# Kernel optimization log

Measured on AMD Instinct MI355X. Metric: run time of the kernel, lower is better.

## Reference

```python
import jax, jax.numpy as jnp
import numpy as np

N, D, C = 8192, 128, 64
MARGIN = 0.5


def setup_inputs() -> dict:
    key = jax.random.key(0)
    k1, k2 = jax.random.split(key)
    embedings = jax.random.normal(k1, (N, D), dtype=jnp.float32)
    targets = jax.random.randint(k2, (N,), 0, C, dtype=jnp.int32)
    return {"embedings": embedings, "targets": targets}


def _triplet_terms(x, targets):
    # pairwise squared distances, faithful to pairwise_distances(y=None):
    xn = jnp.sum(x * x, axis=1)                       # [N]
    d = xn[:, None] + xn[None, :] - 2.0 * (x @ x.T)   # [N, N]
    d = jnp.clip(d - jnp.diagonal(d)[None, :], 0.0)

    same = targets[:, None] == targets[None, :]        # [N, N] bool
    diff = ~same
    BIG = jnp.float32(1e30)
    g_pos = jnp.argmax(jnp.where(same, d, -BIG), axis=1)  # farthest same-class (global idx)
    g_neg = jnp.argmin(jnp.where(diff, d, BIG), axis=1)   # closest other-class (global idx)

    # Faithful to source bug: the mined index is the POSITION WITHIN THE
    # SAME/DIFF-CLASS SUBSET (np.argsort on the masked slice), which the
    # original then uses to index the full embedding batch.
    cum_same = jnp.cumsum(same.astype(jnp.int32), axis=1)
    cum_diff = jnp.cumsum(diff.astype(jnp.int32), axis=1)
    p_pos = jnp.take_along_axis(cum_same, g_pos[:, None], axis=1)[:, 0] - 1
    p_neg = jnp.take_along_axis(cum_diff, g_neg[:, None], axis=1)[:, 0] - 1

    anchors = x
    positives = x[p_pos]
    negatives = x[p_neg]

    valid = (jnp.sum(same, axis=1) > 1) & (jnp.sum(diff, axis=1) >= 1)
    vf = valid.astype(x.dtype)                         # [N]
    vcount = jnp.sum(vf)

    ap = jnp.sum((anchors - positives) ** 2, axis=1)
    an = jnp.sum((anchors - negatives) ** 2, axis=1)
    npd = jnp.sum((positives - negatives) ** 2, axis=1)

    tl = jax.nn.relu(ap - an + MARGIN) * vf
    non_zero = jnp.sum((tl > 0).astype(jnp.int32))
    triplet_term = jnp.where(
        non_zero == 0,
        jnp.sum(tl) / vcount,                                   # mean over valid rows
        jnp.sum(tl) / jnp.maximum(non_zero, 1).astype(x.dtype),  # sum(tl / non_zero)
    )

    l1 = lambda v: jnp.sum(jnp.abs(v) * vf[:, None]) / vcount
    sparse_term = (l1(anchors) + l1(positives) + l1(negatives)) / 3.0

    pairwise_term = jax.nn.relu(jnp.sum((ap - an - npd) * vf) / vcount)

    ap_mean = jnp.sum(ap * vf) / vcount
    an_mean = jnp.sum(an * vf) / vcount
    return triplet_term, sparse_term, pairwise_term, vcount, ap_mean, an_mean


def reference(embedings, targets):
    return _triplet_terms(embedings, targets)
```

## Files before the change

kernel.cpp:

```cpp
#include <hip/hip_runtime.h>
#include <float.h>
#include <stdint.h>

#define NROWS 8192
#define DIM 128
#define MARGIN 0.5f
#define NCHUNK (NROWS / 64)
#define SCH 16
#define RLB (NROWS / 8)

typedef __attribute__((ext_vector_type(8))) short short8;
typedef __attribute__((ext_vector_type(4))) float floatx4;

__device__ __forceinline__ void load_lds16(const void* g, void* l) {
    __builtin_amdgcn_global_load_lds(
        (const __attribute__((address_space(1))) unsigned int*)g,
        (__attribute__((address_space(3))) unsigned int*)l, 16, 0, 0);
}

__device__ __forceinline__ unsigned rne_pack(float v0, float v1) {
    unsigned u0 = __float_as_uint(v0), u1 = __float_as_uint(v1);
    unsigned r0 = (u0 + 0x7fffu + ((u0 >> 16) & 1u)) >> 16;
    unsigned r1 = (u1 + 0x7fffu + ((u1 >> 16) & 1u)) & 0xffff0000u;
    return r0 | r1;
}

__global__ __launch_bounds__(256) void prep_kernel(const float* __restrict__ x,
                                                   const int* __restrict__ tgt,
                                                   uint4* __restrict__ fragH,
                                                   float* __restrict__ xn,
                                                   float* __restrict__ l1n,
                                                   int* __restrict__ pre,
                                                   int* __restrict__ cc,
                                                   float* __restrict__ gacc,
                                                   int* __restrict__ cnt) {
    __shared__ int cntS[NCHUNK][64];
    const int b = blockIdx.x;
    if (b < NROWS / 16) {
        float (*sums)[17] = (float (*)[17])cntS;
        float (*suml)[17] = ((float (*)[17])cntS) + 16;
        const int t = threadIdx.x;
        const int s = t >> 6, lane = t & 63;
        const int rloc = lane & 15;
        const int k0 = s * 32 + (lane >> 4) * 8;
        const float* xr = x + (size_t)(b * 16 + rloc) * DIM + k0;
        float4 va = *(const float4*)xr, vb = *(const float4*)(xr + 4);
        float vv[8] = {va.x, va.y, va.z, va.w, vb.x, vb.y, vb.z, vb.w};
        unsigned h[4];
        float ss = 0.f, ll = 0.f;
        #pragma unroll
        for (int e = 0; e < 4; ++e) {
            ss += vv[2 * e] * vv[2 * e] + vv[2 * e + 1] * vv[2 * e + 1];
            ll += fabsf(vv[2 * e]) + fabsf(vv[2 * e + 1]);
            h[e] = rne_pack(vv[2 * e], vv[2 * e + 1]);
        }
        fragH[(size_t)(b * 4 + s) * 64 + lane] = make_uint4(h[0], h[1], h[2], h[3]);
        const int c16 = s * 4 + (lane >> 4);
        sums[rloc][c16] = ss;
        suml[rloc][c16] = ll;
        __syncthreads();
        if (t < 16) {
            float tot = 0.f;
            #pragma unroll
            for (int c2 = 0; c2 < 16; ++c2) tot += sums[t][c2];
            xn[b * 16 + t] = tot;
        } else if (t < 32) {
            const int tt = t - 16;
            float tot = 0.f;
            #pragma unroll
            for (int c2 = 0; c2 < 16; ++c2) tot += suml[tt][c2];
            l1n[b * 16 + tt] = tot;
        }
    } else {
        const int tid = threadIdx.x;
        for (int f = tid; f < NCHUNK * 64; f += 256) ((int*)cntS)[f] = 0;
        __syncthreads();
        for (int j = tid; j < NROWS; j += 256) atomicAdd(&cntS[j >> 6][tgt[j]], 1);
        __syncthreads();
        if (tid < 128) gacc[tid] = 0.0f;
        if (tid == 0) *cnt = 0;
        if (tid < 64) {
            int run = 0;
            for (int k = 0; k < NCHUNK; ++k) {
                pre[k * 64 + tid] = run;
                run += cntS[k][tid];
            }
            cc[tid] = run;
        }
    }
}

__global__ __launch_bounds__(256, 4) void mine_kernel(const uint4* __restrict__ fragH,
                                                      const int* __restrict__ tgt,
                                                      const float* __restrict__ xn,
                                                      float4* __restrict__ part) {
    __shared__ __align__(16) uint4 Sb[1024];
    __shared__ float xnS[64];
    __shared__ int   tgtS[64];

    const int tid  = threadIdx.x;
    const int lane = tid & 63;
    const int w    = tid >> 6;
    const int m    = lane & 15;
    const int q    = lane >> 4;
    const int ib     = blockIdx.x & 63;
    const int chunk  = blockIdx.x >> 6;
    const int i0     = ib * 128;
    const int jbase0 = chunk * (NROWS / SCH);

    short8 aih[2][4];
    float xni[2]; int ti[2];
    #pragma unroll
    for (int t = 0; t < 2; ++t) {
        const int irow = i0 + w * 32 + t * 16 + m;
        xni[t] = xn[irow];
        ti[t]  = tgt[irow];
        const int itile = (i0 >> 4) + w * 2 + t;
        #pragma unroll
        for (int s = 0; s < 4; ++s)
            aih[t][s] = *(const short8*)&fragH[(size_t)(itile * 4 + s) * 64 + lane];
    }

    float vx[2] = {-FLT_MAX, -FLT_MAX}, vn[2] = {FLT_MAX, FLT_MAX};
    int xj[2] = {0, 0}, nj[2] = {0, 0};

    for (int jt = 0; jt < (NROWS / SCH) / 64; ++jt) {
        const int j0 = jbase0 + jt * 64;
        __syncthreads();
        const char* g = (const char*)(fragH + (size_t)(j0 >> 4) * 256);
        #pragma unroll
        for (int it = 0; it < 4; ++it)
            load_lds16(g + it * 4096 + tid * 16,
                       (char*)Sb + it * 4096 + w * 1024);
        if (tid < 64) { xnS[tid] = xn[j0 + tid]; tgtS[tid] = tgt[j0 + tid]; }
        __syncthreads();

        #pragma unroll
        for (int st = 0; st < 4; ++st) {
            floatx4 acc0 = {0.f, 0.f, 0.f, 0.f};
            floatx4 acc1 = {0.f, 0.f, 0.f, 0.f};
            #pragma unroll
            for (int s = 0; s < 4; ++s) {
                short8 jh = *(const short8*)&Sb[(st * 4 + s) * 64 + lane];
                acc0 = __builtin_amdgcn_mfma_f32_16x16x32_bf16(jh, aih[0][s], acc0, 0, 0, 0);
                acc1 = __builtin_amdgcn_mfma_f32_16x16x32_bf16(jh, aih[1][s], acc1, 0, 0, 0);
            }
            float4 xnj4 = *(const float4*)&xnS[st * 16 + q * 4];
            int4   tj4  = *(const int4*)&tgtS[st * 16 + q * 4];
            const int jb = j0 + st * 16 + q * 4;
            float xnj[4] = {xnj4.x, xnj4.y, xnj4.z, xnj4.w};
            int   tj[4]  = {tj4.x, tj4.y, tj4.z, tj4.w};
            #pragma unroll
            for (int t = 0; t < 2; ++t) {
                floatx4 acc = t ? acc1 : acc0;
                #pragma unroll
                for (int r = 0; r < 4; ++r) {
                    float v = fmaf(-2.0f, acc[r], xnj[r]);
                    if (tj[r] == ti[t]) { if (v > vx[t]) { vx[t] = v; xj[t] = jb + r; } }
                    else                { if (v < vn[t]) { vn[t] = v; nj[t] = jb + r; } }
                }
            }
        }
    }

    #pragma unroll
    for (int t = 0; t < 2; ++t) {
        #pragma unroll
        for (int off = 16; off <= 32; off <<= 1) {
            float ox = __shfl_xor(vx[t], off, 64);
            int   oj = __shfl_xor(xj[t], off, 64);
            if (ox > vx[t] || (ox == vx[t] && oj < xj[t])) { vx[t] = ox; xj[t] = oj; }
            float on = __shfl_xor(vn[t], off, 64);
            int  onj = __shfl_xor(nj[t], off, 64);
            if (on < vn[t] || (on == vn[t] && onj < nj[t])) { vn[t] = on; nj[t] = onj; }
        }
        if (q == 0) {
            const int irow = i0 + w * 32 + t * 16 + m;
            part[(size_t)irow * SCH + chunk] =
                make_float4(fmaxf(xni[t] + vx[t], 0.0f), __int_as_float(xj[t]),
                            fmaxf(xni[t] + vn[t], 0.0f), __int_as_float(nj[t]));
        }
    }
}

__global__ __launch_bounds__(256) void rl_kernel(const float* __restrict__ x,
                                                 const int* __restrict__ tgt,
                                                 const float4* __restrict__ part,
                                                 const int* __restrict__ cc,
                                                 const int* __restrict__ pre,
                                                 const float* __restrict__ l1n,
                                                 float* __restrict__ gacc,
                                                 int* __restrict__ cnt,
                                                 float* __restrict__ out) {
    __shared__ float s_red[4][8];
    __shared__ float olds[8];
    __shared__ int isLast;
    const int tid = threadIdx.x, w = tid >> 6, lane = tid & 63;
    const int r0 = blockIdx.x * 8 + w * 2;
    const int sub = lane >> 4;

    float bx = -FLT_MAX, bn = FLT_MAX;
    int bxj = 0x7fffffff, bnj = 0x7fffffff;
    if (lane < 32) {
        float4 v = part[(size_t)(r0 + sub) * SCH + (lane & 15)];
        bx = v.x; bxj = __float_as_int(v.y);
        bn = v.z; bnj = __float_as_int(v.w);
    }
    #pragma unroll
    for (int off = 1; off <= 8; off <<= 1) {
        float ox = __shfl_xor(bx, off, 64);
        int   oj = __shfl_xor(bxj, off, 64);
        if (ox > bx || (ox == bx && oj < bxj)) { bx = ox; bxj = oj; }
        float on = __shfl_xor(bn, off, 64);
        int  onj = __shfl_xor(bnj, off, 64);
        if (on < bn || (on == bn && onj < bnj)) { bn = on; bnj = onj; }
    }
    const int gp0 = __shfl(bxj, 0, 64),  gn0 = __shfl(bnj, 0, 64);
    const int gp1 = __shfl(bxj, 16, 64), gn1 = __shfl(bnj, 16, 64);
    const int ti0 = tgt[r0], ti1 = tgt[r0 + 1];

    const int tA = tgt[(gp0 & ~63) + lane], tB = tgt[(gn0 & ~63) + lane];
    const int tC = tgt[(gp1 & ~63) + lane], tD = tgt[(gn1 & ~63) + lane];
    const int pA = pre[(gp0 >> 6) * 64 + ti0], pB = pre[(gn0 >> 6) * 64 + ti0];
    const int pC = pre[(gp1 >> 6) * 64 + ti1], pD = pre[(gn1 >> 6) * 64 + ti1];
    const int pp0 = pA + __popcll(__ballot(tA == ti0 && lane < (gp0 & 63)));
    const int sb0 = pB + __popcll(__ballot(tB == ti0 && lane < (gn0 & 63)));
    const int pp1 = pC + __popcll(__ballot(tC == ti1 && lane < (gp1 & 63)));
    const int sb1 = pD + __popcll(__ballot(tD == ti1 && lane < (gn1 & 63)));
    const int pn0 = gn0 - sb0, pn1 = gn1 - sb1;

    const float2 a0 = *(const float2*)(x + (size_t)r0 * DIM + lane * 2);
    const float2 p0 = *(const float2*)(x + (size_t)pp0 * DIM + lane * 2);
    const float2 q0 = *(const float2*)(x + (size_t)pn0 * DIM + lane * 2);
    const float2 a1 = *(const float2*)(x + (size_t)(r0 + 1) * DIM + lane * 2);
    const float2 p1 = *(const float2*)(x + (size_t)pp1 * DIM + lane * 2);
    const float2 q1 = *(const float2*)(x + (size_t)pn1 * DIM + lane * 2);

    float v0 = (a0.x - p0.x) * (a0.x - p0.x) + (a0.y - p0.y) * (a0.y - p0.y);
    float v1 = (a0.x - q0.x) * (a0.x - q0.x) + (a0.y - q0.y) * (a0.y - q0.y);
    float v2 = (p0.x - q0.x) * (p0.x - q0.x) + (p0.y - q0.y) * (p0.y - q0.y);
    float v3 = (a1.x - p1.x) * (a1.x - p1.x) + (a1.y - p1.y) * (a1.y - p1.y);
    float v4 = (a1.x - q1.x) * (a1.x - q1.x) + (a1.y - q1.y) * (a1.y - q1.y);
    float v5 = (p1.x - q1.x) * (p1.x - q1.x) + (p1.y - q1.y) * (p1.y - q1.y);
    #pragma unroll
    for (int off = 32; off > 0; off >>= 1) {
        v0 += __shfl_xor(v0, off, 64);
        v1 += __shfl_xor(v1, off, 64);
        v2 += __shfl_xor(v2, off, 64);
        v3 += __shfl_xor(v3, off, 64);
        v4 += __shfl_xor(v4, off, 64);
        v5 += __shfl_xor(v5, off, 64);
    }

    if (lane == 0) {
        const float l10 = l1n[r0] + l1n[pp0] + l1n[pn0];
        const float l11 = l1n[r0 + 1] + l1n[pp1] + l1n[pn1];
        const int c0 = cc[ti0], c1 = cc[ti1];
        const float vf0 = (c0 > 1) ? 1.0f : 0.0f;
        const float vf1 = (c1 > 1) ? 1.0f : 0.0f;
        const float tl0 = fmaxf(v0 - v1 + MARGIN, 0.0f) * vf0;
        const float tl1 = fmaxf(v3 - v4 + MARGIN, 0.0f) * vf1;
        s_red[w][0] = tl0 + tl1;
        s_red[w][1] = ((tl0 > 0.f) ? 1.f : 0.f) + ((tl1 > 0.f) ? 1.f : 0.f);
        s_red[w][2] = vf0 + vf1;
        s_red[w][3] = l10 * vf0 + l11 * vf1;
        s_red[w][4] = (v0 - v1 - v2) * vf0 + (v3 - v4 - v5) * vf1;
        s_red[w][5] = v0 * vf0 + v3 * vf1;
        s_red[w][6] = v1 * vf0 + v4 * vf1;
    }
    __syncthreads();
    if (tid < 7) {
        float val = s_red[0][tid] + s_red[1][tid] + s_red[2][tid] + s_red[3][tid];
        olds[tid] = atomicAdd(&gacc[tid * 16], val);
    }
    __syncthreads();
    if (tid == 0) isLast = (atomicAdd(cnt, 1) == RLB - 1);
    __syncthreads();
    if (!isLast) return;

    if (tid < 7) olds[tid] = atomicAdd(&gacc[tid * 16], 0.0f);
    __syncthreads();
    if (tid == 0) {
        float tl = olds[0], nz = olds[1], vc = olds[2], l1 = olds[3];
        float pw = olds[4], apS = olds[5], anS = olds[6];
        out[0] = (nz == 0.0f) ? (tl / vc) : (tl / fmaxf(nz, 1.0f));
        out[1] = (l1 / vc) * (1.0f / 3.0f);
        out[2] = fmaxf(pw / vc, 0.0f);
        out[3] = vc;
        out[4] = apS / vc;
        out[5] = anS / vc;
    }
}

extern "C" void kernel_launch(void* const* d_in, const int* in_sizes, int n_in,
                              void* d_out, int out_size, void* d_ws, size_t ws_size,
                              hipStream_t stream) {
    const float* x   = (const float*)d_in[0];
    const int*   tgt = (const int*)d_in[1];
    float* out = (float*)d_out;
    char*  ws  = (char*)d_ws;

    size_t off = 0;
    uint4* fragH = (uint4*)ws;                  off += (size_t)NROWS * DIM * 2;
    float* xn    = (float*)(ws + off);          off += (size_t)NROWS * 4;
    float* l1n   = (float*)(ws + off);          off += (size_t)NROWS * 4;
    int*   pre   = (int*)(ws + off);            off += (size_t)NCHUNK * 64 * 4;
    int*   cc    = (int*)(ws + off);            off += 64 * 4;
    float* gacc  = (float*)(ws + off);          off += 128 * 4;
    int*   cnt   = (int*)(ws + off);            off += 64;
    float4* part = (float4*)(ws + off);         off += (size_t)NROWS * SCH * 16;

    prep_kernel<<<NROWS / 16 + 1, 256, 0, stream>>>(x, tgt, fragH, xn, l1n,
                                                    pre, cc, gacc, cnt);
    mine_kernel<<<64 * SCH, 256, 0, stream>>>(fragH, tgt, xn, part);
    rl_kernel<<<RLB, 256, 0, stream>>>(x, tgt, part, cc, pre, l1n, gacc, cnt, out);
}
```

Baseline: 131.1 us.

## Fold class-mask into MFMA via augmented K and pack index into distance bits

Extends the bf16 fragments with 64 extra one-hot class columns so the matmul itself adds a large offset (+/-) for same-class pairs, removing per-element target compares and branches. Argmin/argmax are then tracked as unsigned min/max on float bits with the low 7 bits replaced by a local index, replacing compare-and-select pairs. The cross-block atomic reduction with a last-block flag is replaced by per-block partials and a separate single-block final kernel. This costs 50% more MFMA work and LDS traffic, and truncating mantissa bits may change tie-breaking and the precision of the mined distances.

New measurement: 112.3 us. 1.17x faster.

```diff
diff --git a/kernel.cpp b/kernel.cpp
--- a/kernel.cpp
+++ b/kernel.cpp
@@ -4,6 +4,7 @@
 
 #define NROWS 8192
 #define DIM 128
+#define KAUG 192
 #define MARGIN 0.5f
 #define NCHUNK (NROWS / 64)
 #define SCH 16
@@ -27,13 +28,12 @@
 
 __global__ __launch_bounds__(256) void prep_kernel(const float* __restrict__ x,
                                                    const int* __restrict__ tgt,
-                                                   uint4* __restrict__ fragH,
+                                                   uint4* __restrict__ fragA,
+                                                   uint4* __restrict__ fragB,
                                                    float* __restrict__ xn,
                                                    float* __restrict__ l1n,
                                                    int* __restrict__ pre,
-                                                   int* __restrict__ cc,
-                                                   float* __restrict__ gacc,
-                                                   int* __restrict__ cnt) {
+                                                   int* __restrict__ cc) {
     __shared__ int cntS[NCHUNK][64];
     const int b = blockIdx.x;
     if (b < NROWS / 16) {
@@ -41,8 +41,8 @@
         float (*suml)[17] = ((float (*)[17])cntS) + 16;
         const int t = threadIdx.x;
         const int s = t >> 6, lane = t & 63;
-        const int rloc = lane & 15;
-        const int k0 = s * 32 + (lane >> 4) * 8;
+        const int rloc = lane & 15, q = lane >> 4;
+        const int k0 = s * 32 + q * 8;
         const float* xr = x + (size_t)(b * 16 + rloc) * DIM + k0;
         float4 va = *(const float4*)xr, vb = *(const float4*)(xr + 4);
         float vv[8] = {va.x, va.y, va.z, va.w, vb.x, vb.y, vb.z, vb.w};
@@ -54,8 +54,26 @@
             ll += fabsf(vv[2 * e]) + fabsf(vv[2 * e + 1]);
             h[e] = rne_pack(vv[2 * e], vv[2 * e + 1]);
         }
-        fragH[(size_t)(b * 4 + s) * 64 + lane] = make_uint4(h[0], h[1], h[2], h[3]);
-        const int c16 = s * 4 + (lane >> 4);
+        uint4 hv = make_uint4(h[0], h[1], h[2], h[3]);
+        fragA[(size_t)(b * 6 + s) * 64 + lane] = hv;
+        fragB[(size_t)(b * 6 + s) * 64 + lane] = hv;
+        {
+            const int ab = t >> 6;
+            const unsigned bits = (ab < 2) ? 0x4200u : 0xC200u;
+            const int ti = tgt[b * 16 + rloc];
+            const int cb = (ab & 1) * 32 + q * 8;
+            unsigned hh[4];
+            #pragma unroll
+            for (int e = 0; e < 4; ++e) {
+                unsigned lo = (cb + 2 * e == ti) ? bits : 0u;
+                unsigned hi = (cb + 2 * e + 1 == ti) ? bits : 0u;
+                hh[e] = lo | (hi << 16);
+            }
+            uint4* dst = (ab < 2) ? fragA : fragB;
+            dst[(size_t)(b * 6 + 4 + (ab & 1)) * 64 + lane] =
+                make_uint4(hh[0], hh[1], hh[2], hh[3]);
+        }
+        const int c16 = s * 4 + q;
         sums[rloc][c16] = ss;
         suml[rloc][c16] = ll;
         __syncthreads();
@@ -77,8 +95,6 @@
         __syncthreads();
         for (int j = tid; j < NROWS; j += 256) atomicAdd(&cntS[j >> 6][tgt[j]], 1);
         __syncthreads();
-        if (tid < 128) gacc[tid] = 0.0f;
-        if (tid == 0) *cnt = 0;
         if (tid < 64) {
             int run = 0;
             for (int k = 0; k < NCHUNK; ++k) {
@@ -90,13 +106,12 @@
     }
 }
 
-__global__ __launch_bounds__(256, 4) void mine_kernel(const uint4* __restrict__ fragH,
-                                                      const int* __restrict__ tgt,
+__global__ __launch_bounds__(256, 4) void mine_kernel(const uint4* __restrict__ fragA,
+                                                      const uint4* __restrict__ fragB,
                                                       const float* __restrict__ xn,
                                                       float4* __restrict__ part) {
-    __shared__ __align__(16) uint4 Sb[1024];
+    __shared__ __align__(16) uint4 Sb[1536];
     __shared__ float xnS[64];
-    __shared__ int   tgtS[64];
 
     const int tid  = threadIdx.x;
     const int lane = tid & 63;
@@ -108,31 +123,31 @@
     const int i0     = ib * 128;
     const int jbase0 = chunk * (NROWS / SCH);
 
-    short8 aih[2][4];
-    float xni[2]; int ti[2];
+    short8 aih[2][6];
+    float xni[2];
     #pragma unroll
     for (int t = 0; t < 2; ++t) {
         const int irow = i0 + w * 32 + t * 16 + m;
         xni[t] = xn[irow];
-        ti[t]  = tgt[irow];
         const int itile = (i0 >> 4) + w * 2 + t;
         #pragma unroll
-        for (int s = 0; s < 4; ++s)
-            aih[t][s] = *(const short8*)&fragH[(size_t)(itile * 4 + s) * 64 + lane];
-    }
-
-    float vx[2] = {-FLT_MAX, -FLT_MAX}, vn[2] = {FLT_MAX, FLT_MAX};
-    int xj[2] = {0, 0}, nj[2] = {0, 0};
+        for (int s = 0; s < 6; ++s)
+            aih[t][s] = *(const short8*)&fragA[(size_t)(itile * 6 + s) * 64 + lane];
+    }
+
+    unsigned kmin[2] = {0xFFFFFFFFu, 0xFFFFFFFFu};
+    unsigned kmax[2] = {0u, 0u};
+    const unsigned M = 0xFFFFFF80u;
 
     for (int jt = 0; jt < (NROWS / SCH) / 64; ++jt) {
         const int j0 = jbase0 + jt * 64;
         __syncthreads();
-        const char* g = (const char*)(fragH + (size_t)(j0 >> 4) * 256);
-        #pragma unroll
-        for (int it = 0; it < 4; ++it)
+        const char* g = (const char*)fragB + (size_t)(j0 >> 4) * 6144;
+        #pragma unroll
+        for (int it = 0; it < 6; ++it)
             load_lds16(g + it * 4096 + tid * 16,
                        (char*)Sb + it * 4096 + w * 1024);
-        if (tid < 64) { xnS[tid] = xn[j0 + tid]; tgtS[tid] = tgt[j0 + tid]; }
+        if (tid < 64) xnS[tid] = xn[j0 + tid] + 1024.0f;
         __syncthreads();
 
         #pragma unroll
@@ -140,24 +155,23 @@
             floatx4 acc0 = {0.f, 0.f, 0.f, 0.f};
             floatx4 acc1 = {0.f, 0.f, 0.f, 0.f};
             #pragma unroll
-            for (int s = 0; s < 4; ++s) {
-                short8 jh = *(const short8*)&Sb[(st * 4 + s) * 64 + lane];
+            for (int s = 0; s < 6; ++s) {
+                short8 jh = *(const short8*)&Sb[(st * 6 + s) * 64 + lane];
                 acc0 = __builtin_amdgcn_mfma_f32_16x16x32_bf16(jh, aih[0][s], acc0, 0, 0, 0);
                 acc1 = __builtin_amdgcn_mfma_f32_16x16x32_bf16(jh, aih[1][s], acc1, 0, 0, 0);
             }
             float4 xnj4 = *(const float4*)&xnS[st * 16 + q * 4];
-            int4   tj4  = *(const int4*)&tgtS[st * 16 + q * 4];
-            const int jb = j0 + st * 16 + q * 4;
             float xnj[4] = {xnj4.x, xnj4.y, xnj4.z, xnj4.w};
-            int   tj[4]  = {tj4.x, tj4.y, tj4.z, tj4.w};
             #pragma unroll
             for (int t = 0; t < 2; ++t) {
                 floatx4 acc = t ? acc1 : acc0;
                 #pragma unroll
                 for (int r = 0; r < 4; ++r) {
+                    const unsigned e = (unsigned)(jt * 16 + st * 4 + r);
                     float v = fmaf(-2.0f, acc[r], xnj[r]);
-                    if (tj[r] == ti[t]) { if (v > vx[t]) { vx[t] = v; xj[t] = jb + r; } }
-                    else                { if (v < vn[t]) { vn[t] = v; nj[t] = jb + r; } }
+                    unsigned u = __float_as_uint(v);
+                    kmin[t] = min(kmin[t], (u & M) | e);
+                    kmax[t] = max(kmax[t], (u & M) | (127u - e));
                 }
             }
         }
@@ -165,20 +179,26 @@
 
     #pragma unroll
     for (int t = 0; t < 2; ++t) {
+        unsigned e1 = kmin[t] & 127u;
+        float dmin = xni[t] + (__uint_as_float(kmin[t] & M) - 1024.0f);
+        int jmin = jbase0 + (int)((e1 >> 4) * 64 + ((e1 >> 2) & 3) * 16) + q * 4 + (int)(e1 & 3);
+        unsigned e2 = 127u - (kmax[t] & 127u);
+        float dmax = xni[t] + (__uint_as_float(kmax[t] & M) - 3072.0f);
+        int jmax = jbase0 + (int)((e2 >> 4) * 64 + ((e2 >> 2) & 3) * 16) + q * 4 + (int)(e2 & 3);
+
         #pragma unroll
         for (int off = 16; off <= 32; off <<= 1) {
-            float ox = __shfl_xor(vx[t], off, 64);
-            int   oj = __shfl_xor(xj[t], off, 64);
-            if (ox > vx[t] || (ox == vx[t] && oj < xj[t])) { vx[t] = ox; xj[t] = oj; }
-            float on = __shfl_xor(vn[t], off, 64);
-            int  onj = __shfl_xor(nj[t], off, 64);
-            if (on < vn[t] || (on == vn[t] && onj < nj[t])) { vn[t] = on; nj[t] = onj; }
+            float ox = __shfl_xor(dmax, off, 64);
+            int   oj = __shfl_xor(jmax, off, 64);
+            if (ox > dmax || (ox == dmax && oj < jmax)) { dmax = ox; jmax = oj; }
+            float on = __shfl_xor(dmin, off, 64);
+            int  onj = __shfl_xor(jmin, off, 64);
+            if (on < dmin || (on == dmin && onj < jmin)) { dmin = on; jmin = onj; }
         }
         if (q == 0) {
             const int irow = i0 + w * 32 + t * 16 + m;
             part[(size_t)irow * SCH + chunk] =
-                make_float4(fmaxf(xni[t] + vx[t], 0.0f), __int_as_float(xj[t]),
-                            fmaxf(xni[t] + vn[t], 0.0f), __int_as_float(nj[t]));
+                make_float4(dmax, __int_as_float(jmax), dmin, __int_as_float(jmin));
         }
     }
 }
@@ -189,12 +209,8 @@
                                                  const int* __restrict__ cc,
                                                  const int* __restrict__ pre,
                                                  const float* __restrict__ l1n,
-                                                 float* __restrict__ gacc,
-                                                 int* __restrict__ cnt,
-                                                 float* __restrict__ out) {
+                                                 float* __restrict__ bp) {
     __shared__ float s_red[4][8];
-    __shared__ float olds[8];
-    __shared__ int isLast;
     const int tid = threadIdx.x, w = tid >> 6, lane = tid & 63;
     const int r0 = blockIdx.x * 8 + w * 2;
     const int sub = lane >> 4;
@@ -269,20 +285,29 @@
         s_red[w][6] = v1 * vf0 + v4 * vf1;
     }
     __syncthreads();
-    if (tid < 7) {
-        float val = s_red[0][tid] + s_red[1][tid] + s_red[2][tid] + s_red[3][tid];
-        olds[tid] = atomicAdd(&gacc[tid * 16], val);
-    }
-    __syncthreads();
-    if (tid == 0) isLast = (atomicAdd(cnt, 1) == RLB - 1);
-    __syncthreads();
-    if (!isLast) return;
-
-    if (tid < 7) olds[tid] = atomicAdd(&gacc[tid * 16], 0.0f);
+    if (tid < 8)
+        bp[blockIdx.x * 8 + tid] =
+            s_red[0][tid] + s_red[1][tid] + s_red[2][tid] + s_red[3][tid];
+}
+
+__global__ __launch_bounds__(256) void final_kernel(const float* __restrict__ bp,
+                                                    float* __restrict__ out) {
+    __shared__ float red[32][8];
+    const int tid = threadIdx.x, k = tid & 7;
+    float s = 0.0f;
+    for (int i = tid >> 3; i < RLB; i += 32) s += bp[i * 8 + k];
+    red[tid >> 3][k] = s;
     __syncthreads();
     if (tid == 0) {
-        float tl = olds[0], nz = olds[1], vc = olds[2], l1 = olds[3];
-        float pw = olds[4], apS = olds[5], anS = olds[6];
+        float tot[7];
+        #pragma unroll
+        for (int kk = 0; kk < 7; ++kk) {
+            float t = 0.0f;
+            for (int i = 0; i < 32; ++i) t += red[i][kk];
+            tot[kk] = t;
+        }
+        float tl = tot[0], nz = tot[1], vc = tot[2], l1 = tot[3];
+        float pw = tot[4], apS = tot[5], anS = tot[6];
         out[0] = (nz == 0.0f) ? (tl / vc) : (tl / fmaxf(nz, 1.0f));
         out[1] = (l1 / vc) * (1.0f / 3.0f);
         out[2] = fmaxf(pw / vc, 0.0f);
@@ -300,18 +325,20 @@
     float* out = (float*)d_out;
     char*  ws  = (char*)d_ws;
 
+    const size_t fragBytes = (size_t)NROWS * KAUG * 2;
     size_t off = 0;
-    uint4* fragH = (uint4*)ws;                  off += (size_t)NROWS * DIM * 2;
+    uint4* fragA = (uint4*)ws;                  off += fragBytes;
+    uint4* fragB = (uint4*)(ws + off);          off += fragBytes;
     float* xn    = (float*)(ws + off);          off += (size_t)NROWS * 4;
     float* l1n   = (float*)(ws + off);          off += (size_t)NROWS * 4;
     int*   pre   = (int*)(ws + off);            off += (size_t)NCHUNK * 64 * 4;
     int*   cc    = (int*)(ws + off);            off += 64 * 4;
-    float* gacc  = (float*)(ws + off);          off += 128 * 4;
-    int*   cnt   = (int*)(ws + off);            off += 64;
+    float* bp    = (float*)(ws + off);          off += (size_t)RLB * 8 * 4;
     float4* part = (float4*)(ws + off);         off += (size_t)NROWS * SCH * 16;
 
-    prep_kernel<<<NROWS / 16 + 1, 256, 0, stream>>>(x, tgt, fragH, xn, l1n,
-                                                    pre, cc, gacc, cnt);
-    mine_kernel<<<64 * SCH, 256, 0, stream>>>(fragH, tgt, xn, part);
-    rl_kernel<<<RLB, 256, 0, stream>>>(x, tgt, part, cc, pre, l1n, gacc, cnt, out);
-}
+    prep_kernel<<<NROWS / 16 + 1, 256, 0, stream>>>(x, tgt, fragA, fragB,
+                                                    xn, l1n, pre, cc);
+    mine_kernel<<<64 * SCH, 256, 0, stream>>>(fragA, fragB, xn, part);
+    rl_kernel<<<RLB, 256, 0, stream>>>(x, tgt, part, cc, pre, l1n, bp);
+    final_kernel<<<1, 256, 0, stream>>>(bp, out);
+}
```
